# Kernel tuning notes

Measured on AMD Instinct MI355X. Metric: run time of the kernel, lower is better.

The kernel has to match this reference:

```python
import jax, jax.numpy as jnp
import numpy as np
import math

# ---- model constants (match init_kwargs) ----
B, T, HID = 2, 4096, 2048
H, D = 16, 128            # heads, head_dim; num_kv_heads == H
ROPE_DIM = 64             # head_dim * partial_rotary_factor (0.5)
THETA = 10000.0
EPS = 1e-6
CHUNK = 64                # chunk size for the chunked simple-GLA scan
LAYER_IDX, N_LAYERS = 12, 32


def _alibi_slopes(n):
    # power-of-2 path of build_slope_tensor
    start = 2.0 ** (-(2.0 ** -(math.log2(n) - 3.0)))
    return np.array([start ** (i + 1) for i in range(n)], dtype=np.float32)


def _layer_slope():
    scale = 1.0 - (LAYER_IDX - 1) / (N_LAYERS - 1) + 1e-5
    return jnp.asarray(-_alibi_slopes(H) * scale)  # [H], negative log-decay per step


def _rmsnorm(x, w):
    xf = x.astype(jnp.float32)
    var = jnp.mean(xf * xf, axis=-1, keepdims=True)
    return (w * (xf * jax.lax.rsqrt(var + EPS)).astype(x.dtype))


def _group_rmsnorm(x, w, groups):
    # x: [..., groups*gd]; normalize within each group, then elementwise weight
    shp = x.shape
    xg = x.reshape(shp[:-1] + (groups, shp[-1] // groups)).astype(jnp.float32)
    var = jnp.mean(xg * xg, axis=-1, keepdims=True)
    xn = (xg * jax.lax.rsqrt(var + EPS)).astype(x.dtype).reshape(shp)
    return w * xn


def _rope_cos_sin(position_ids):
    inv_freq = 1.0 / (THETA ** (jnp.arange(0, ROPE_DIM, 2, dtype=jnp.float32) / ROPE_DIM))
    freqs = position_ids.astype(jnp.float32)[..., None] * inv_freq  # [B,T,ROPE_DIM/2]
    emb = jnp.concatenate([freqs, freqs], axis=-1)                  # [B,T,ROPE_DIM]
    return jnp.cos(emb), jnp.sin(emb)


def _rotate_half(x):
    x1, x2 = jnp.split(x, 2, axis=-1)
    return jnp.concatenate([-x2, x1], axis=-1)


def _apply_rope(x, cos, sin):
    # x: [B,T,H,D]; partial rotary on first ROPE_DIM dims
    c = cos[:, :, None, :]
    s = sin[:, :, None, :]
    x_rot, x_pass = x[..., :ROPE_DIM], x[..., ROPE_DIM:]
    x_rot = x_rot * c + _rotate_half(x_rot) * s
    return jnp.concatenate([x_rot, x_pass], axis=-1)


def _chunk_simple_gla(q, k, v, slope):
    # q,k,v: [B,T,H,D]; slope: [H] (negative per-step log-decay)
    # recurrence: S_t = exp(slope)*S_{t-1} + k_t^T v_t ; o_t = q_t S_t
    q = q * (D ** -0.5)
    nc = T // CHUNK
    def to_chunks(x):
        # [B,T,H,D] -> [nc,B,H,CHUNK,D]
        return x.reshape(B, nc, CHUNK, H, D).transpose(1, 0, 3, 2, 4)
    qc, kc, vc = to_chunks(q), to_chunks(k), to_chunks(v)

    i = jnp.arange(CHUNK, dtype=jnp.float32)
    g = slope[:, None, None]                                  # [H,1,1]
    mask = jnp.where(i[:, None] >= i[None, :],
                     jnp.exp(g * (i[:, None] - i[None, :])), 0.0)   # [H,C,C]
    q_dec = jnp.exp(slope[:, None] * (i + 1.0))               # [H,C]
    k_dec = jnp.exp(slope[:, None] * (CHUNK - 1.0 - i))       # [H,C]
    ch_dec = jnp.exp(slope * CHUNK)                           # [H]

    S0 = jnp.zeros((B, H, D, D), q.dtype)

    def step(S, inp):
        qi, ki, vi = inp                                       # [B,H,C,D]
        att = jnp.einsum('bhcd,bhed->bhce', qi, ki) * mask[None]
        intra = jnp.einsum('bhce,bhed->bhcd', att, vi)
        inter = jnp.einsum('bhcd,bhde->bhce', qi * q_dec[None, :, :, None], S)
        S_new = ch_dec[None, :, None, None] * S + \
            jnp.einsum('bhcd,bhce->bhde', ki * k_dec[None, :, :, None], vi)
        return S_new, intra + inter

    _, o = jax.lax.scan(step, S0, (qc, kc, vc))                # o: [nc,B,H,C,D]
    return o.transpose(1, 0, 3, 2, 4).reshape(B, T, H * D)


def setup_inputs() -> dict:
    key = jax.random.key(0)
    ks = jax.random.split(key, 4)
    return {
        'hidden_states': jax.random.normal(ks[0], (B, T, HID), jnp.float32),
        'w_qkv': jax.random.normal(ks[1], (3 * H * D, HID), jnp.float32) * 0.02,
        'q_ln_w': jnp.ones((D,), jnp.float32),
        'k_ln_w': jnp.ones((D,), jnp.float32),
        'g_norm_w': jnp.ones((H * D,), jnp.float32),
        'w_g_proj': jax.random.normal(ks[2], (H * D, HID), jnp.float32) * 0.02,
        'w_dense': jax.random.normal(ks[3], (HID, H * D), jnp.float32) * 0.02,
        'position_ids': jnp.arange(B * T, dtype=jnp.int32).reshape(B, T) % T,
    }


def reference(hidden_states, w_qkv, q_ln_w, k_ln_w, g_norm_w, w_g_proj, w_dense, position_ids):
    slope = _layer_slope()
    qkv = jnp.einsum('bth,oh->bto', hidden_states, w_qkv)
    q, k, v = jnp.split(qkv, [H * D, 2 * H * D], axis=-1)
    q = q.reshape(B, T, H, D)
    k = k.reshape(B, T, H, D)
    v = v.reshape(B, T, H, D)
    # qk-norm (per-head RMSNorm)
    q = _rmsnorm(q, q_ln_w)
    k = _rmsnorm(k, k_ln_w)
    # partial RoPE
    cos, sin = _rope_cos_sin(position_ids)
    q = _apply_rope(q, cos, sin)
    k = _apply_rope(k, cos, sin)
    # chunked lightning (simple-GLA) linear attention
    o = _chunk_simple_gla(q, k, v, slope)                      # [B,T,H*D]
    # group RMSNorm (per head) + sigmoid output gate, then output proj
    gate = jax.nn.sigmoid(jnp.einsum('bth,oh->bto', hidden_states, w_g_proj))
    o = _group_rmsnorm(o, g_norm_w, groups=H) * gate
    return jnp.einsum('bto,ho->bth', o, w_dense)
```

## Files before the change

### kernel.cpp

```cpp
#include <hip/hip_runtime.h>
#include <math.h>

typedef short bf16x8 __attribute__((ext_vector_type(8)));
typedef float f32x4 __attribute__((ext_vector_type(4)));

#define LOG2E 1.4426950408889634f
#define GSCALE 0.6451712903225806f

__device__ __forceinline__ float bf2f(unsigned short h) {
    union { unsigned u; float f; } v; v.u = ((unsigned)h) << 16; return v.f;
}
__device__ __forceinline__ unsigned short f2bf(float f) {
    union { float f; unsigned u; } v; v.f = f;
    unsigned r = v.u + 0x7FFFu + ((v.u >> 16) & 1u);
    return (unsigned short)(r >> 16);
}

#define GLD16(lds, g)                                                          \
    __builtin_amdgcn_global_load_lds(                                          \
        (const __attribute__((address_space(1))) void*)(g),                    \
        (__attribute__((address_space(3))) void*)(lds), 16, 0, 0)

#define MFMA16(a, b, c) __builtin_amdgcn_mfma_f32_16x16x32_bf16(a, b, c, 0, 0, 0)

struct us4 { unsigned short a, b, c, d; };
__global__ __launch_bounds__(256) void cvt4_f32_bf16(
    const float* __restrict__ s0, const float* __restrict__ s1,
    const float* __restrict__ s2, const float* __restrict__ s3,
    unsigned short* __restrict__ dst, int c0, int c1, int c2, int n4)
{
    int i = blockIdx.x * 256 + threadIdx.x;
    if (i >= n4) return;
    const float* s; int off;
    if (i < c0)      { s = s0; off = i; }
    else if (i < c1) { s = s1; off = i - c0; }
    else if (i < c2) { s = s2; off = i - c1; }
    else             { s = s3; off = i - c2; }
    float4 v = ((const float4*)s)[off];
    us4 o = { f2bf(v.x), f2bf(v.y), f2bf(v.z), f2bf(v.w) };
    ((us4*)dst)[i] = o;
}

template <int EPI>
__global__ __launch_bounds__(512, 2) void gemm256(
    const unsigned short* __restrict__ A, const unsigned short* __restrict__ Bt,
    void* __restrict__ Cv,
    unsigned short* __restrict__ Qp, unsigned short* __restrict__ Kp,
    unsigned short* __restrict__ Vp, unsigned short* __restrict__ Gb,
    int M, int N, int K)
{
    __shared__ __attribute__((aligned(16))) unsigned short lA[2][16384];
    __shared__ __attribute__((aligned(16))) unsigned short lB[2][16384];

    const int tid  = threadIdx.x;
    const int lane = tid & 63, wave = tid >> 6;
    const int quad = lane >> 4, lr = lane & 15;
    const int wm   = (wave >> 2) * 128;
    const int wn   = (wave & 3) * 64;
    const int lsw  = lr & 7;

    const int lin = (int)(blockIdx.y * gridDim.x + blockIdx.x);
    const int xcd = lin & 7, j = lin >> 3;
    const int RPC = (int)gridDim.y >> 3;
    const int bm  = xcd * RPC + (j % RPC);
    const int bn  = j / RPC;

    const unsigned short* Ab = A  + (long long)bm * 256 * K;
    const unsigned short* Bb = Bt + (long long)bn * 256 * K;

    const int c0r = tid, c1r = 512 + tid;
    const int row0 = c0r >> 3, row1 = c1r >> 3;
    const long long ga0 = (long long)row0 * K + ((c0r & 7) ^ (row0 & 7)) * 8;
    const long long ga1 = (long long)row1 * K + ((c1r & 7) ^ (row1 & 7)) * 8;
    const long long HK  = (long long)128 * K;
    const int l0 = c0r * 8, l1 = c1r * 8;

#define STAGE(ldsb, gb, half, kt)                                              \
    do {                                                                       \
        GLD16((ldsb) + (half) * 8192 + l0, (gb) + (half) * HK + (kt) + ga0);   \
        GLD16((ldsb) + (half) * 8192 + l1, (gb) + (half) * HK + (kt) + ga1);   \
    } while (0)

    f32x4 acc[8][4] = {};
    bf16x8 a[4][2], blo[2][2], bhi[2][2];

#define LOADA(buf, base)                                                       \
    _Pragma("unroll") for (int i = 0; i < 4; ++i)                              \
    _Pragma("unroll") for (int s = 0; s < 2; ++s)                              \
        a[i][s] = *(const bf16x8*)((buf) + ((base) + i * 16 + lr) * 64 +       \
                                   (((s * 4 + quad) ^ lsw) * 8));
#define LOADB(dst, buf, base)                                                  \
    _Pragma("unroll") for (int j2 = 0; j2 < 2; ++j2)                           \
    _Pragma("unroll") for (int s = 0; s < 2; ++s)                              \
        dst[j2][s] = *(const bf16x8*)((buf) + ((base) + j2 * 16 + lr) * 64 +   \
                                      (((s * 4 + quad) ^ lsw) * 8));
#define MFMAQ(MQ, NQ, BV)                                                      \
    _Pragma("unroll") for (int i = 0; i < 4; ++i)                              \
    _Pragma("unroll") for (int j2 = 0; j2 < 2; ++j2)                           \
    _Pragma("unroll") for (int s = 0; s < 2; ++s)                              \
        acc[(MQ) * 4 + i][(NQ) * 2 + j2] =                                     \
            MFMA16(a[i][s], BV[j2][s], acc[(MQ) * 4 + i][(NQ) * 2 + j2]);

#define BARR()  asm volatile("s_barrier" ::: "memory")
#define LGKM0() asm volatile("s_waitcnt lgkmcnt(0)" ::: "memory")
#define VM4()   asm volatile("s_waitcnt vmcnt(4)" ::: "memory")
#define VM6()   asm volatile("s_waitcnt vmcnt(6)" ::: "memory")
#define SBAR()  __builtin_amdgcn_sched_barrier(0)
#define PBEG()  do { BARR(); LGKM0(); SBAR();                                  \
                     __builtin_amdgcn_s_setprio(1); } while (0)
#define PBEGW(W) do { W(); BARR(); SBAR();                                     \
                     __builtin_amdgcn_s_setprio(1); } while (0)
#define PEND()  do { SBAR(); __builtin_amdgcn_s_setprio(0); BARR(); } while (0)

    STAGE(lA[0], Ab, 0, 0); STAGE(lA[0], Ab, 1, 0);
    STAGE(lB[0], Bb, 0, 0); STAGE(lB[0], Bb, 1, 0);
    STAGE(lB[1], Bb, 0, 64); STAGE(lB[1], Bb, 1, 64);
    STAGE(lA[1], Ab, 0, 64);
    VM6();
    BARR();

    const int NT = K >> 6;
    for (int it = 0; it < (NT >> 1); ++it) {
        const int v   = 2 * it + 1;
        const int kn0 = (2 * it + 2 < NT) ? (2 * it + 2) * 64 : 0;
        const int kn1 = (2 * it + 3 < NT) ? (2 * it + 3) * 64 : 0;
        LOADA(lA[0], wm); LOADB(blo, lB[0], wn);
        STAGE(lA[1], Ab, 1, v * 64);
        PBEG(); MFMAQ(0, 0, blo); PEND();
        LOADB(bhi, lB[0], wn + 32);
        PBEG(); MFMAQ(0, 1, bhi); PEND();
        LOADA(lA[0], wm + 64);
        STAGE(lB[0], Bb, 0, kn0);
        PBEG(); MFMAQ(1, 1, bhi); PEND();
        STAGE(lB[0], Bb, 1, kn0);
        PBEGW(VM4); MFMAQ(1, 0, blo); PEND();
        LOADA(lA[1], wm); LOADB(blo, lB[1], wn);
        STAGE(lA[0], Ab, 0, kn0);
        PBEG(); MFMAQ(0, 0, blo); PEND();
        LOADB(bhi, lB[1], wn + 32);
        STAGE(lA[0], Ab, 1, kn0);
        PBEG(); MFMAQ(0, 1, bhi); PEND();
        LOADA(lA[1], wm + 64);
        STAGE(lB[1], Bb, 0, kn1);
        PBEG(); MFMAQ(1, 1, bhi); PEND();
        STAGE(lB[1], Bb, 1, kn1); STAGE(lA[1], Ab, 0, kn1);
        PBEGW(VM6); MFMAQ(1, 0, blo); PEND();
    }
    asm volatile("s_waitcnt vmcnt(0)" ::: "memory");

#pragma unroll
    for (int i = 0; i < 8; ++i)
#pragma unroll
        for (int j2 = 0; j2 < 4; ++j2)
#pragma unroll
            for (int r = 0; r < 4; ++r) {
                int row = bm * 256 + wm + i * 16 + quad * 4 + r;
                int col = bn * 256 + wn + j2 * 16 + lr;
                float vv = acc[i][j2][r];
                if (EPI == 0) {
                    if (col < 6144) {
                        int tens = col >> 11, h = (col >> 7) & 15, e = col & 127;
                        int b = row >> 12, t = row & 4095;
                        long long dst = (((long long)(b * 16 + h)) * 4096 + t) * 128 + e;
                        unsigned short* P = (tens == 0) ? Qp : ((tens == 1) ? Kp : Vp);
                        P[dst] = f2bf(vv);
                    } else {
                        vv = 1.0f / (1.0f + __expf(-vv));
                        Gb[(long long)row * 2048 + (col - 6144)] = f2bf(vv);
                    }
                } else {
                    ((float*)Cv)[(long long)row * N + col] = vv;
                }
            }
#undef STAGE
#undef LOADA
#undef LOADB
#undef MFMAQ
#undef BARR
#undef LGKM0
#undef VM4
#undef VM6
#undef SBAR
#undef PBEG
#undef PBEGW
#undef PEND
}

__global__ __launch_bounds__(256) void norm_rope(
    unsigned short* __restrict__ Qp, unsigned short* __restrict__ Kp,
    const float* __restrict__ qw, const float* __restrict__ kw,
    const int* __restrict__ pos_ids)
{
    const int bid  = blockIdx.x;
    const int tg   = bid & 1023, h = (bid >> 10) & 15, b = bid >> 14;
    const int wave = threadIdx.x >> 6, lane = threadIdx.x & 63;
    const int t    = tg * 4 + wave;
    const long long rowbase = (((long long)(b * 16 + h)) * 4096 + t) * 128;
    const int pos = pos_ids[b * 4096 + t];
    const int d0  = lane * 2;

    float c0 = 1.f, s0 = 0.f, c1 = 1.f, s1 = 0.f;
    if (lane < 32) {
        float fj0 = (float)(d0 & 31), fj1 = (float)((d0 + 1) & 31);
        float if0 = exp2f(-fj0 * 0.4152410118609203f);
        float if1 = exp2f(-fj1 * 0.4152410118609203f);
        sincosf((float)pos * if0, &s0, &c0);
        sincosf((float)pos * if1, &s1, &c1);
    }
    const float w0q = qw[d0], w1q = qw[d0 + 1];
    const float w0k = kw[d0], w1k = kw[d0 + 1];

#pragma unroll
    for (int which = 0; which < 2; ++which) {
        unsigned short* P = which ? Kp : Qp;
        float w0 = which ? w0k : w0q, w1 = which ? w1k : w1q;
        unsigned u = *(const unsigned*)(P + rowbase + d0);
        float x0 = bf2f(u & 0xFFFF), x1 = bf2f(u >> 16);
        float ss = x0 * x0 + x1 * x1;
#pragma unroll
        for (int off = 32; off; off >>= 1) ss += __shfl_xor(ss, off);
        float r  = rsqrtf(ss * (1.0f / 128.0f) + 1e-6f);
        float xn0 = x0 * r * w0;
        float xn1 = x1 * r * w1;
        float p0 = __shfl_xor(xn0, 16);
        float p1 = __shfl_xor(xn1, 16);
        float y0, y1;
        if (d0 < 32)      { y0 = xn0 * c0 - p0 * s0; y1 = xn1 * c1 - p1 * s1; }
        else if (d0 < 64) { y0 = xn0 * c0 + p0 * s0; y1 = xn1 * c1 + p1 * s1; }
        else              { y0 = xn0; y1 = xn1; }
        if (which == 0) { y0 *= 0.08838834764831845f; y1 *= 0.08838834764831845f; }
        *(unsigned*)(P + rowbase + d0) =
            (unsigned)f2bf(y0) | ((unsigned)f2bf(y1) << 16);
    }
}

__global__ __launch_bounds__(256) void gla_chunk(
    const unsigned short* __restrict__ Qp, const unsigned short* __restrict__ Kp,
    const unsigned short* __restrict__ Vp,
    unsigned short* __restrict__ Oint, unsigned short* __restrict__ Ubuf)
{
    __shared__ __attribute__((aligned(16))) unsigned short sK[64 * 136];
    __shared__ __attribute__((aligned(16))) unsigned short sVT[128 * 72];
    __shared__ __attribute__((aligned(16))) unsigned short sKT[128 * 72];
    __shared__ __attribute__((aligned(16))) unsigned short sAtt[64 * 72];

    const int bid = blockIdx.x;
    const int n = bid & 63, h = (bid >> 6) & 15, b = bid >> 10;
    const int tid = threadIdx.x, wave = tid >> 6, lane = tid & 63;
    const int quad = lane >> 4, lr = lane & 15;
    const float gl2 = -exp2f(-0.5f * (float)(h + 1)) * GSCALE * LOG2E;

    const long long rb = (((long long)(b * 16 + h)) * 4096 + (long long)n * 64) * 128;

    const int cS = wave * 16 + lr;
    const float qsc = exp2f(gl2 * (float)cS);
    bf16x8 qf[4];
#pragma unroll
    for (int ks = 0; ks < 4; ++ks) {
        union { uint4 v; unsigned short s[8]; } in, ou;
        in.v = *(const uint4*)(Qp + rb + cS * 128 + ks * 32 + quad * 8);
#pragma unroll
        for (int j = 0; j < 8; ++j) ou.s[j] = f2bf(bf2f(in.s[j]) * qsc);
        qf[ks] = *(bf16x8*)&ou;
    }
#pragma unroll
    for (int rr = 0; rr < 4; ++rr) {
        int idx = rr * 256 + tid;
        int c = idx >> 4, d8 = (idx & 15) << 3;
        *(uint4*)(sK + c * 136 + d8) = *(const uint4*)(Kp + rb + c * 128 + d8);
    }
#pragma unroll
    for (int rr = 0; rr < 4; ++rr) {
        int idx = rr * 256 + tid;
        int c = idx & 63, g8 = (idx >> 6) << 3;
        union { uint4 v; unsigned short s[8]; } vv, kk;
        vv.v = *(const uint4*)(Vp + rb + c * 128 + g8);
        kk.v = *(const uint4*)(Kp + rb + c * 128 + g8);
        float kdsc = exp2f(gl2 * (float)(64 - c));
#pragma unroll
        for (int j = 0; j < 8; ++j) {
            sVT[(g8 + j) * 72 + c] = vv.s[j];
            sKT[(g8 + j) * 72 + c] = f2bf(bf2f(kk.s[j]) * kdsc);
        }
    }
    __syncthreads();

    f32x4 aacc[4] = {};
#pragma unroll
    for (int nj = 0; nj < 4; ++nj)
#pragma unroll
        for (int ks = 0; ks < 4; ++ks) {
            bf16x8 bf = *(const bf16x8*)(sK + (nj * 16 + lr) * 136 + ks * 32 + quad * 8);
            aacc[nj] = MFMA16(qf[ks], bf, aacc[nj]);
        }
#pragma unroll
    for (int nj = 0; nj < 4; ++nj) {
        int c2 = nj * 16 + lr;
        float colf = exp2f(-gl2 * (float)c2);
#pragma unroll
        for (int r = 0; r < 4; ++r) {
            int c = wave * 16 + quad * 4 + r;
            sAtt[c * 72 + c2] = f2bf((c >= c2) ? aacc[nj][r] * colf : 0.0f);
        }
    }
    f32x4 Sacc[2][8] = {};
#pragma unroll
    for (int me = 0; me < 2; ++me)
#pragma unroll
        for (int ks = 0; ks < 2; ++ks) {
            bf16x8 af = *(const bf16x8*)(sVT + (wave * 32 + me * 16 + lr) * 72 + ks * 32 + quad * 8);
#pragma unroll
            for (int dj = 0; dj < 8; ++dj) {
                bf16x8 bf = *(const bf16x8*)(sKT + (dj * 16 + lr) * 72 + ks * 32 + quad * 8);
                Sacc[me][dj] = MFMA16(af, bf, Sacc[me][dj]);
            }
        }
    const long long ub = ((long long)((b * 16 + h) * 64 + n)) * 16384;
#pragma unroll
    for (int me = 0; me < 2; ++me)
#pragma unroll
        for (int r = 0; r < 4; ++r) {
            int e = wave * 32 + me * 16 + quad * 4 + r;
#pragma unroll
            for (int dj = 0; dj < 8; ++dj)
                Ubuf[ub + e * 128 + dj * 16 + lr] = f2bf(Sacc[me][dj][r]);
        }
    __syncthreads();

    f32x4 oacc[8] = {};
#pragma unroll
    for (int ks = 0; ks < 2; ++ks) {
        bf16x8 af = *(const bf16x8*)(sAtt + cS * 72 + ks * 32 + quad * 8);
#pragma unroll
        for (int ej = 0; ej < 8; ++ej) {
            bf16x8 bf = *(const bf16x8*)(sVT + (ej * 16 + lr) * 72 + ks * 32 + quad * 8);
            oacc[ej] = MFMA16(af, bf, oacc[ej]);
        }
    }
#pragma unroll
    for (int ej = 0; ej < 8; ++ej)
#pragma unroll
        for (int r = 0; r < 4; ++r) {
            int c = wave * 16 + quad * 4 + r;
            long long off = ((long long)(b * 4096 + n * 64 + c)) * 2048 + h * 128 + ej * 16 + lr;
            Oint[off] = f2bf(oacc[ej][r]);
        }
}

__global__ __launch_bounds__(256) void gla_scan(
    const unsigned short* __restrict__ Ubuf, unsigned short* __restrict__ STbuf)
{
    const int bid = blockIdx.x;
    const int es = bid & 7, bh = bid >> 3;
    const int h = bh & 15;
    const float gl2 = -exp2f(-0.5f * (float)(h + 1)) * GSCALE * LOG2E;
    const float chd = exp2f(gl2 * 64.0f);
    const int tid = threadIdx.x;
    const long long base = (long long)bh * 64 * 16384 + es * 2048 + tid * 8;
    float st[8] = {};
    for (int n = 0; n < 64; ++n) {
        long long a = base + (long long)n * 16384;
        union { uint4 v; unsigned short s[8]; } u, o;
        u.v = *(const uint4*)(Ubuf + a);
#pragma unroll
        for (int j = 0; j < 8; ++j) o.s[j] = f2bf(st[j]);
        *(uint4*)(STbuf + a) = o.v;
#pragma unroll
        for (int j = 0; j < 8; ++j) st[j] = st[j] * chd + bf2f(u.s[j]);
    }
}

__global__ __launch_bounds__(256) void gla_inter(
    const unsigned short* __restrict__ Qp, const unsigned short* __restrict__ STbuf,
    unsigned short* __restrict__ Ob, const unsigned short* __restrict__ Gb,
    const float* __restrict__ W)
{
    __shared__ __attribute__((aligned(16))) unsigned short sST[128 * 136];
    const int bid = blockIdx.x;
    const int n = bid & 63, h = (bid >> 6) & 15, b = bid >> 10;
    const int tid = threadIdx.x, wave = tid >> 6, lane = tid & 63;
    const int quad = lane >> 4, lr = lane & 15;
    const float gl2 = -exp2f(-0.5f * (float)(h + 1)) * GSCALE * LOG2E;
    const long long rb = (((long long)(b * 16 + h)) * 4096 + (long long)n * 64) * 128;
    const long long stb = ((long long)((b * 16 + h) * 64 + n)) * 16384;

#pragma unroll
    for (int rr = 0; rr < 8; ++rr) {
        int idx = rr * 256 + tid;
        int row = idx >> 4, d8 = (idx & 15) << 3;
        *(uint4*)(sST + row * 136 + d8) = *(const uint4*)(STbuf + stb + row * 128 + d8);
    }
    const int cS = wave * 16 + lr;
    const float qsc = exp2f(gl2 * (float)cS);
    bf16x8 qf[4];
#pragma unroll
    for (int ks = 0; ks < 4; ++ks) {
        union { uint4 v; unsigned short s[8]; } in, ou;
        in.v = *(const uint4*)(Qp + rb + cS * 128 + ks * 32 + quad * 8);
#pragma unroll
        for (int j = 0; j < 8; ++j) ou.s[j] = f2bf(bf2f(in.s[j]) * qsc);
        qf[ks] = *(bf16x8*)&ou;
    }
    __syncthreads();

    f32x4 oacc[8] = {};
#pragma unroll
    for (int ks = 0; ks < 4; ++ks)
#pragma unroll
        for (int ej = 0; ej < 8; ++ej) {
            bf16x8 bf = *(const bf16x8*)(sST + (ej * 16 + lr) * 136 + ks * 32 + quad * 8);
            oacc[ej] = MFMA16(qf[ks], bf, oacc[ej]);
        }

    float w[8];
#pragma unroll
    for (int ej = 0; ej < 8; ++ej) w[ej] = W[h * 128 + ej * 16 + lr];

    float ss[4] = {};
#pragma unroll
    for (int r = 0; r < 4; ++r) {
        int c = wave * 16 + quad * 4 + r;
        long long off = ((long long)(b * 4096 + n * 64 + c)) * 2048 + h * 128;
#pragma unroll
        for (int ej = 0; ej < 8; ++ej) {
            float v = oacc[ej][r] + bf2f(Ob[off + ej * 16 + lr]);
            oacc[ej][r] = v;
            ss[r] += v * v;
        }
    }
#pragma unroll
    for (int r = 0; r < 4; ++r) {
#pragma unroll
        for (int o2 = 1; o2 < 16; o2 <<= 1) ss[r] += __shfl_xor(ss[r], o2);
        float rn = rsqrtf(ss[r] * (1.0f / 128.0f) + 1e-6f);
        int c = wave * 16 + quad * 4 + r;
        long long off = ((long long)(b * 4096 + n * 64 + c)) * 2048 + h * 128;
#pragma unroll
        for (int ej = 0; ej < 8; ++ej) {
            float g = bf2f(Gb[off + ej * 16 + lr]);
            Ob[off + ej * 16 + lr] = f2bf(oacc[ej][r] * rn * w[ej] * g);
        }
    }
}

extern "C" void kernel_launch(void* const* d_in, const int* in_sizes, int n_in,
                              void* d_out, int out_size, void* d_ws, size_t ws_size,
                              hipStream_t stream)
{
    const float* hid   = (const float*)d_in[0];
    const float* w_qkv = (const float*)d_in[1];
    const float* q_ln  = (const float*)d_in[2];
    const float* k_ln  = (const float*)d_in[3];
    const float* g_nw  = (const float*)d_in[4];
    const float* w_g   = (const float*)d_in[5];
    const float* w_d   = (const float*)d_in[6];
    const int*   pos   = (const int*)d_in[7];

    const size_t PLANE = (size_t)2 * 16 * 4096 * 128;
    unsigned short* Qp    = (unsigned short*)d_ws;
    unsigned short* Kp    = Qp + PLANE;
    unsigned short* Vp    = Kp + PLANE;
    unsigned short* Ob    = Vp + PLANE;
    unsigned short* Gb    = Ob + PLANE;
    unsigned short* hidb  = Gb + PLANE;
    unsigned short* wqkvb = hidb + (size_t)8192 * 2048;
    unsigned short* wgb   = wqkvb + (size_t)6144 * 2048;
    unsigned short* wdb   = wgb + (size_t)2048 * 2048;
    unsigned short* Ubuf  = hidb;
    unsigned short* STbuf = Kp;

    dim3 blk(256);
    const int c0 = 8192 * 2048 / 4;
    const int c1 = c0 + 6144 * 2048 / 4;
    const int c2 = c1 + 2048 * 2048 / 4;
    const int n4 = c2 + 2048 * 2048 / 4;
    cvt4_f32_bf16<<<(n4 + 255) / 256, blk, 0, stream>>>(
        hid, w_qkv, w_g, w_d, hidb, c0, c1, c2, n4);

    gemm256<0><<<dim3(32, 32), dim3(512), 0, stream>>>(
        hidb, wqkvb, nullptr, Qp, Kp, Vp, Gb, 8192, 8192, 2048);
    norm_rope<<<32768, blk, 0, stream>>>(Qp, Kp, q_ln, k_ln, pos);
    gla_chunk<<<2048, blk, 0, stream>>>(Qp, Kp, Vp, Ob, Ubuf);
    gla_scan<<<256, blk, 0, stream>>>(Ubuf, STbuf);
    gla_inter<<<2048, blk, 0, stream>>>(Qp, STbuf, Ob, Gb, g_nw);
    gemm256<2><<<dim3(8, 32), dim3(512), 0, stream>>>(
        Ob, wdb, d_out, nullptr, nullptr, nullptr, nullptr, 8192, 2048, 2048);
}
```

Measured before the change: 634.9 us.

## Restructure GEMM main loop with register double-buffered fragments and fewer barriers

The GEMM main loop is rewritten. The old schedule used many small MFMA quadrants, each wrapped in its own barrier pair and interleaved with half-tile global-to-LDS stages. The new one loads full 8x4 fragment sets per 32-wide k-slice into two register buffers and alternates them, so LDS reads for the next slice overlap the current MFMA cluster. Whole A/B tiles are staged with four 16-byte loads per thread. This cuts the number of s_barriers and waitcnts per iteration, but uses more VGPRs and gives a coarser overlap between global loads and compute.

```diff
diff --git a/kernel.cpp b/kernel.cpp
--- a/kernel.cpp
+++ b/kernel.cpp
@@ -68,83 +68,63 @@
     const unsigned short* Ab = A  + (long long)bm * 256 * K;
     const unsigned short* Bb = Bt + (long long)bn * 256 * K;
 
-    const int c0r = tid, c1r = 512 + tid;
-    const int row0 = c0r >> 3, row1 = c1r >> 3;
-    const long long ga0 = (long long)row0 * K + ((c0r & 7) ^ (row0 & 7)) * 8;
-    const long long ga1 = (long long)row1 * K + ((c1r & 7) ^ (row1 & 7)) * 8;
-    const long long HK  = (long long)128 * K;
-    const int l0 = c0r * 8, l1 = c1r * 8;
-
-#define STAGE(ldsb, gb, half, kt)                                              \
-    do {                                                                       \
-        GLD16((ldsb) + (half) * 8192 + l0, (gb) + (half) * HK + (kt) + ga0);   \
-        GLD16((ldsb) + (half) * 8192 + l1, (gb) + (half) * HK + (kt) + ga1);   \
-    } while (0)
+    const int r0 = tid >> 3, g0 = tid & 7;
+    const long long gbase = (long long)r0 * K + ((g0 ^ (r0 & 7)) * 8);
+    const int lbase = tid * 8;
+
+#define STAGE4(lds, gb, kt)                                                    \
+    _Pragma("unroll") for (int w = 0; w < 4; ++w)                              \
+        GLD16((lds) + w * 4096 + lbase,                                        \
+              (gb) + (long long)w * 64 * K + (kt) + gbase);
 
     f32x4 acc[8][4] = {};
-    bf16x8 a[4][2], blo[2][2], bhi[2][2];
-
-#define LOADA(buf, base)                                                       \
-    _Pragma("unroll") for (int i = 0; i < 4; ++i)                              \
-    _Pragma("unroll") for (int s = 0; s < 2; ++s)                              \
-        a[i][s] = *(const bf16x8*)((buf) + ((base) + i * 16 + lr) * 64 +       \
-                                   (((s * 4 + quad) ^ lsw) * 8));
-#define LOADB(dst, buf, base)                                                  \
-    _Pragma("unroll") for (int j2 = 0; j2 < 2; ++j2)                           \
-    _Pragma("unroll") for (int s = 0; s < 2; ++s)                              \
-        dst[j2][s] = *(const bf16x8*)((buf) + ((base) + j2 * 16 + lr) * 64 +   \
-                                      (((s * 4 + quad) ^ lsw) * 8));
-#define MFMAQ(MQ, NQ, BV)                                                      \
-    _Pragma("unroll") for (int i = 0; i < 4; ++i)                              \
-    _Pragma("unroll") for (int j2 = 0; j2 < 2; ++j2)                           \
-    _Pragma("unroll") for (int s = 0; s < 2; ++s)                              \
-        acc[(MQ) * 4 + i][(NQ) * 2 + j2] =                                     \
-            MFMA16(a[i][s], BV[j2][s], acc[(MQ) * 4 + i][(NQ) * 2 + j2]);
+    bf16x8 a0[8], b0[4], a1[8], b1[4];
+
+#define LDA8(F, buf, s)                                                        \
+    _Pragma("unroll") for (int i = 0; i < 8; ++i)                              \
+        F[i] = *(const bf16x8*)((buf) + (wm + i * 16 + lr) * 64 +              \
+                                ((((s) * 4 + quad) ^ lsw) * 8));
+#define LDB4(F, buf, s)                                                        \
+    _Pragma("unroll") for (int j2 = 0; j2 < 4; ++j2)                           \
+        F[j2] = *(const bf16x8*)((buf) + (wn + j2 * 16 + lr) * 64 +            \
+                                 ((((s) * 4 + quad) ^ lsw) * 8));
+#define MFMAS(FA, FB)                                                          \
+    _Pragma("unroll") for (int i = 0; i < 8; ++i)                              \
+    _Pragma("unroll") for (int j2 = 0; j2 < 4; ++j2)                           \
+        acc[i][j2] = MFMA16(FA[i], FB[j2], acc[i][j2]);
 
 #define BARR()  asm volatile("s_barrier" ::: "memory")
 #define LGKM0() asm volatile("s_waitcnt lgkmcnt(0)" ::: "memory")
-#define VM4()   asm volatile("s_waitcnt vmcnt(4)" ::: "memory")
-#define VM6()   asm volatile("s_waitcnt vmcnt(6)" ::: "memory")
+#define VM8()   asm volatile("s_waitcnt vmcnt(8)" ::: "memory")
 #define SBAR()  __builtin_amdgcn_sched_barrier(0)
-#define PBEG()  do { BARR(); LGKM0(); SBAR();                                  \
-                     __builtin_amdgcn_s_setprio(1); } while (0)
-#define PBEGW(W) do { W(); BARR(); SBAR();                                     \
-                     __builtin_amdgcn_s_setprio(1); } while (0)
-#define PEND()  do { SBAR(); __builtin_amdgcn_s_setprio(0); BARR(); } while (0)
-
-    STAGE(lA[0], Ab, 0, 0); STAGE(lA[0], Ab, 1, 0);
-    STAGE(lB[0], Bb, 0, 0); STAGE(lB[0], Bb, 1, 0);
-    STAGE(lB[1], Bb, 0, 64); STAGE(lB[1], Bb, 1, 64);
-    STAGE(lA[1], Ab, 0, 64);
-    VM6();
+#define MCLUST(FA, FB)                                                         \
+    do { SBAR(); __builtin_amdgcn_s_setprio(1); MFMAS(FA, FB);                 \
+         __builtin_amdgcn_s_setprio(0); SBAR(); } while (0)
+
+    STAGE4(lA[0], Ab, 0);  STAGE4(lB[0], Bb, 0);
+    STAGE4(lA[1], Ab, 64); STAGE4(lB[1], Bb, 64);
+    VM8();
     BARR();
+    LDA8(a0, lA[0], 0); LDB4(b0, lB[0], 0);
 
     const int NT = K >> 6;
     for (int it = 0; it < (NT >> 1); ++it) {
-        const int v   = 2 * it + 1;
-        const int kn0 = (2 * it + 2 < NT) ? (2 * it + 2) * 64 : 0;
-        const int kn1 = (2 * it + 3 < NT) ? (2 * it + 3) * 64 : 0;
-        LOADA(lA[0], wm); LOADB(blo, lB[0], wn);
-        STAGE(lA[1], Ab, 1, v * 64);
-        PBEG(); MFMAQ(0, 0, blo); PEND();
-        LOADB(bhi, lB[0], wn + 32);
-        PBEG(); MFMAQ(0, 1, bhi); PEND();
-        LOADA(lA[0], wm + 64);
-        STAGE(lB[0], Bb, 0, kn0);
-        PBEG(); MFMAQ(1, 1, bhi); PEND();
-        STAGE(lB[0], Bb, 1, kn0);
-        PBEGW(VM4); MFMAQ(1, 0, blo); PEND();
-        LOADA(lA[1], wm); LOADB(blo, lB[1], wn);
-        STAGE(lA[0], Ab, 0, kn0);
-        PBEG(); MFMAQ(0, 0, blo); PEND();
-        LOADB(bhi, lB[1], wn + 32);
-        STAGE(lA[0], Ab, 1, kn0);
-        PBEG(); MFMAQ(0, 1, bhi); PEND();
-        LOADA(lA[1], wm + 64);
-        STAGE(lB[1], Bb, 0, kn1);
-        PBEG(); MFMAQ(1, 1, bhi); PEND();
-        STAGE(lB[1], Bb, 1, kn1); STAGE(lA[1], Ab, 0, kn1);
-        PBEGW(VM6); MFMAQ(1, 0, blo); PEND();
+        const int knu = (2 * it + 2 < NT) ? (2 * it + 2) * 64 : 0;
+        const int knv = (2 * it + 3 < NT) ? (2 * it + 3) * 64 : 0;
+        LDA8(a1, lA[0], 1); LDB4(b1, lB[0], 1);
+        MCLUST(a0, b0);
+        LGKM0(); BARR();
+        STAGE4(lA[0], Ab, knu); STAGE4(lB[0], Bb, knu);
+        VM8(); BARR();
+        LDA8(a0, lA[1], 0); LDB4(b0, lB[1], 0);
+        MCLUST(a1, b1);
+        LDA8(a1, lA[1], 1); LDB4(b1, lB[1], 1);
+        MCLUST(a0, b0);
+        LGKM0(); BARR();
+        STAGE4(lA[1], Ab, knv); STAGE4(lB[1], Bb, knv);
+        VM8(); BARR();
+        LDA8(a0, lA[0], 0); LDB4(b0, lB[0], 0);
+        MCLUST(a1, b1);
     }
     asm volatile("s_waitcnt vmcnt(0)" ::: "memory");
 
@@ -172,18 +152,15 @@
                     ((float*)Cv)[(long long)row * N + col] = vv;
                 }
             }
-#undef STAGE
-#undef LOADA
-#undef LOADB
-#undef MFMAQ
+#undef STAGE4
+#undef LDA8
+#undef LDB4
+#undef MFMAS
 #undef BARR
 #undef LGKM0
-#undef VM4
-#undef VM6
+#undef VM8
 #undef SBAR
-#undef PBEG
-#undef PBEGW
-#undef PEND
+#undef MCLUST
 }
 
 __global__ __launch_bounds__(256) void norm_rope(
```

Result: no change. 626.1 us (-1.4%).
